# Optimization experiments

Measured on AMD Instinct MI355X. Metric: run time of the kernel, lower is better.

## Reference

```python
import jax, jax.numpy as jnp
import numpy as np

BSZ, IN_DIM, HID, OUT_DIM, N_ITERS = 262144, 64, 128, 64, 30


def setup_inputs() -> dict:
    key = jax.random.key(0)
    ks = jax.random.split(key, 6)
    s_h = 1.0 / np.sqrt(HID)
    s_i = 1.0 / np.sqrt(IN_DIM)
    return {
        "x": jax.random.normal(ks[0], (BSZ, IN_DIM), dtype=jnp.float32),
        "Wz": jax.random.uniform(ks[1], (HID, HID), jnp.float32, -s_h, s_h) * 0.9,  # scaled for contraction
        "Ux": jax.random.uniform(ks[2], (HID, IN_DIM), jnp.float32, -s_i, s_i),
        "b": jax.random.uniform(ks[3], (HID,), jnp.float32, -s_h, s_h),
        "Wd": jax.random.uniform(ks[4], (OUT_DIM, HID), jnp.float32, -s_h, s_h),
        "bd": jax.random.uniform(ks[5], (OUT_DIM,), jnp.float32, -s_h, s_h),
        "n_iters": N_ITERS,
    }


def reference(x, Wz, Ux, b, Wd, bd, n_iters):
    # injection term is iteration-invariant: compute once
    inj = x @ Ux.T + b                     # [B, HID]
    z0 = jnp.zeros((x.shape[0], Wz.shape[0]), dtype=x.dtype)

    def step(z, _):
        z = jax.nn.relu(z @ Wz.T + inj)    # f(z, x)
        return z, None

    z_star, _ = jax.lax.scan(step, z0, None, length=n_iters)
    return z_star @ Wd.T + bd              # decoder Linear
```

## Files before the change

### kernel.cpp

```cpp
#include <hip/hip_runtime.h>


typedef __attribute__((ext_vector_type(8))) __bf16 bf16x8;
typedef __attribute__((ext_vector_type(4))) __bf16 bf16x4;
typedef __attribute__((ext_vector_type(4))) float  floatx4;

#define MFMA16(a, b, c) __builtin_amdgcn_mfma_f32_16x16x32_bf16((a), (b), (c), 0, 0, 0)

static constexpr int kBsz = 262144;
static constexpr int kTM  = 64;

__device__ __forceinline__ bf16x8 cvt_bf16x8(float4 a, float4 b) {
  bf16x8 r;
  r[0] = (__bf16)a.x; r[1] = (__bf16)a.y; r[2] = (__bf16)a.z; r[3] = (__bf16)a.w;
  r[4] = (__bf16)b.x; r[5] = (__bf16)b.y; r[6] = (__bf16)b.z; r[7] = (__bf16)b.w;
  return r;
}

__global__ void __launch_bounds__(256) deq_fused(
    const float* __restrict__ x,
    const float* __restrict__ Wz,
    const float* __restrict__ Ux,
    const float* __restrict__ bvec,
    const float* __restrict__ Wd,
    const float* __restrict__ bd,
    const int*  __restrict__ n_iters_p,
    float* __restrict__ out)
{
  __shared__ __align__(16) __bf16 zl[2][kTM][136];

  const int tid  = threadIdx.x;
  const int lane = tid & 63;
  const int wv   = tid >> 6;
  const int wn   = wv & 1;
  const int wm   = wv >> 1;
  const int l15  = lane & 15;
  const int quad = lane >> 4;
  const int row0 = blockIdx.x * kTM;
  const int iters = *n_iters_p;

  bf16x8 awz[4][4];
#pragma unroll
  for (int nt = 0; nt < 4; ++nt) {
    const int n = 64 * wn + 16 * nt + l15;
#pragma unroll
    for (int ks = 0; ks < 4; ++ks) {
      const float4* p = (const float4*)(Wz + n * 128 + 32 * ks + 8 * quad);
      awz[nt][ks] = cvt_bf16x8(p[0], p[1]);
    }
  }

  floatx4 inj[4][2];
#pragma unroll
  for (int nt = 0; nt < 4; ++nt) {
    const float4 bv = *(const float4*)(bvec + 64 * wn + 16 * nt + 4 * quad);
#pragma unroll
    for (int mt = 0; mt < 2; ++mt) {
      floatx4 v = {bv.x, bv.y, bv.z, bv.w};
      inj[nt][mt] = v;
    }
  }
  {
    bf16x8 aux[4][2];
#pragma unroll
    for (int nt = 0; nt < 4; ++nt) {
      const int n = 64 * wn + 16 * nt + l15;
#pragma unroll
      for (int ks = 0; ks < 2; ++ks) {
        const float4* p = (const float4*)(Ux + n * 64 + 32 * ks + 8 * quad);
        aux[nt][ks] = cvt_bf16x8(p[0], p[1]);
      }
    }
#pragma unroll
    for (int mt = 0; mt < 2; ++mt) {
      const int m = row0 + 32 * wm + 16 * mt + l15;
#pragma unroll
      for (int ks = 0; ks < 2; ++ks) {
        const float4* p = (const float4*)(x + m * 64 + 32 * ks + 8 * quad);
        const bf16x8 bx = cvt_bf16x8(p[0], p[1]);
#pragma unroll
        for (int nt = 0; nt < 4; ++nt)
          inj[nt][mt] = MFMA16(aux[nt][ks], bx, inj[nt][mt]);
      }
    }
  }

#pragma unroll
  for (int mt = 0; mt < 2; ++mt) {
    const int ml = 32 * wm + 16 * mt + l15;
#pragma unroll
    for (int nt = 0; nt < 4; ++nt) {
      bf16x4 z4;
#pragma unroll
      for (int i = 0; i < 4; ++i) z4[i] = (__bf16)fmaxf(inj[nt][mt][i], 0.0f);
      *(bf16x4*)&zl[0][ml][64 * wn + 16 * nt + 4 * quad] = z4;
    }
  }

  int pb = 0;
  for (int t = 0; t < iters - 1; ++t) {
    __syncthreads();
    bf16x8 bz[2][4];
#pragma unroll
    for (int mt = 0; mt < 2; ++mt) {
      const int ml = 32 * wm + 16 * mt + l15;
#pragma unroll
      for (int ks = 0; ks < 4; ++ks)
        bz[mt][ks] = *(const bf16x8*)&zl[pb][ml][32 * ks + 8 * quad];
    }
    const int nb = pb ^ 1;
#pragma unroll
    for (int mt = 0; mt < 2; ++mt) {
      const int ml = 32 * wm + 16 * mt + l15;
#pragma unroll
      for (int nt = 0; nt < 4; ++nt) {
        floatx4 acc = inj[nt][mt];
#pragma unroll
        for (int ks = 0; ks < 4; ++ks)
          acc = MFMA16(awz[nt][ks], bz[mt][ks], acc);
        bf16x4 z4;
#pragma unroll
        for (int i = 0; i < 4; ++i) z4[i] = (__bf16)fmaxf(acc[i], 0.0f);
        *(bf16x4*)&zl[nb][ml][64 * wn + 16 * nt + 4 * quad] = z4;
      }
    }
    pb = nb;
  }
  __syncthreads();

  bf16x8 awd[2][4];
#pragma unroll
  for (int ot = 0; ot < 2; ++ot) {
    const int o = 32 * wn + 16 * ot + l15;
#pragma unroll
    for (int ks = 0; ks < 4; ++ks) {
      const float4* p = (const float4*)(Wd + o * 128 + 32 * ks + 8 * quad);
      awd[ot][ks] = cvt_bf16x8(p[0], p[1]);
    }
  }
#pragma unroll
  for (int mt = 0; mt < 2; ++mt) {
    const int ml = 32 * wm + 16 * mt + l15;
    bf16x8 bz[4];
#pragma unroll
    for (int ks = 0; ks < 4; ++ks)
      bz[ks] = *(const bf16x8*)&zl[pb][ml][32 * ks + 8 * quad];
#pragma unroll
    for (int ot = 0; ot < 2; ++ot) {
      const float4 bv = *(const float4*)(bd + 32 * wn + 16 * ot + 4 * quad);
      floatx4 acc = {bv.x, bv.y, bv.z, bv.w};
#pragma unroll
      for (int ks = 0; ks < 4; ++ks)
        acc = MFMA16(awd[ot][ks], bz[ks], acc);
      float4 ov;
      ov.x = acc[0]; ov.y = acc[1]; ov.z = acc[2]; ov.w = acc[3];
      *(float4*)(out + (size_t)(row0 + ml) * 64 + 32 * wn + 16 * ot + 4 * quad) = ov;
    }
  }
}

extern "C" void kernel_launch(void* const* d_in, const int* in_sizes, int n_in,
                              void* d_out, int out_size, void* d_ws, size_t ws_size,
                              hipStream_t stream) {
  const float* x  = (const float*)d_in[0];
  const float* Wz = (const float*)d_in[1];
  const float* Ux = (const float*)d_in[2];
  const float* b  = (const float*)d_in[3];
  const float* Wd = (const float*)d_in[4];
  const float* bd = (const float*)d_in[5];
  const int* n_it = (const int*)d_in[6];
  float* out = (float*)d_out;
  (void)in_sizes; (void)n_in; (void)d_ws; (void)ws_size; (void)out_size;

  dim3 grid(kBsz / kTM);
  deq_fused<<<grid, 256, 0, stream>>>(x, Wz, Ux, b, Wd, bd, n_it, out);
}
```

Before: 346.9 us.

## Keep DEQ state in registers per wave using permlane swaps instead of LDS

Each wave now owns 16 batch rows and the full 128-wide hidden state, so the iterate never leaves registers. The MFMA output layout is turned back into the B-operand layout with v_permlane32_swap and ds_swizzle, which removes the shared-memory round trip and the __syncthreads in each of the 30 iterations. In exchange each wave holds all of Wz in registers (32 bf16x8), which raises register pressure and may lower occupancy. It also gives up the 2x2 wave tiling in which each wave reused its Wz slice across 32 rows.

```diff
diff --git a/kernel.cpp b/kernel.cpp
--- a/kernel.cpp
+++ b/kernel.cpp
@@ -2,19 +2,46 @@
 
 
 typedef __attribute__((ext_vector_type(8))) __bf16 bf16x8;
-typedef __attribute__((ext_vector_type(4))) __bf16 bf16x4;
+typedef __attribute__((ext_vector_type(2))) __bf16 bf16x2;
 typedef __attribute__((ext_vector_type(4))) float  floatx4;
 
 #define MFMA16(a, b, c) __builtin_amdgcn_mfma_f32_16x16x32_bf16((a), (b), (c), 0, 0, 0)
 
 static constexpr int kBsz = 262144;
-static constexpr int kTM  = 64;
 
 __device__ __forceinline__ bf16x8 cvt_bf16x8(float4 a, float4 b) {
   bf16x8 r;
   r[0] = (__bf16)a.x; r[1] = (__bf16)a.y; r[2] = (__bf16)a.z; r[3] = (__bf16)a.w;
   r[4] = (__bf16)b.x; r[5] = (__bf16)b.y; r[6] = (__bf16)b.z; r[7] = (__bf16)b.w;
   return r;
+}
+
+__device__ __forceinline__ unsigned pk_relu2(float a, float b) {
+  union { bf16x2 h; unsigned u; } x;
+  x.h[0] = (__bf16)fmaxf(a, 0.0f);
+  x.h[1] = (__bf16)fmaxf(b, 0.0f);
+  return x.u;
+}
+
+union Frag { bf16x8 v; unsigned w[4]; };
+
+__device__ __forceinline__ bf16x8 build_frag(unsigned ulo, unsigned vlo,
+                                             unsigned uhi, unsigned vhi,
+                                             bool qodd) {
+  asm("v_permlane32_swap_b32 %0, %1" : "+v"(ulo), "+v"(vlo));
+  asm("v_permlane32_swap_b32 %0, %1" : "+v"(uhi), "+v"(vhi));
+  const unsigned c0 = qodd ? vlo : ulo;
+  const unsigned d0 = qodd ? ulo : vlo;
+  const unsigned c1 = qodd ? vhi : uhi;
+  const unsigned d1 = qodd ? uhi : vhi;
+  const unsigned dx0 = __builtin_amdgcn_ds_swizzle((int)d0, 0x401F);
+  const unsigned dx1 = __builtin_amdgcn_ds_swizzle((int)d1, 0x401F);
+  Frag f;
+  f.w[0] = qodd ? dx0 : c0;
+  f.w[1] = qodd ? dx1 : c1;
+  f.w[2] = qodd ? c0 : dx0;
+  f.w[3] = qodd ? c1 : dx1;
+  return f.v;
 }
 
 __global__ void __launch_bounds__(256) deq_fused(
@@ -27,135 +54,97 @@
     const int*  __restrict__ n_iters_p,
     float* __restrict__ out)
 {
-  __shared__ __align__(16) __bf16 zl[2][kTM][136];
-
   const int tid  = threadIdx.x;
   const int lane = tid & 63;
   const int wv   = tid >> 6;
-  const int wn   = wv & 1;
-  const int wm   = wv >> 1;
   const int l15  = lane & 15;
   const int quad = lane >> 4;
-  const int row0 = blockIdx.x * kTM;
-  const int iters = *n_iters_p;
+  const bool qodd = (quad & 1) != 0;
+  const int  mrow = blockIdx.x * 64 + wv * 16 + l15;
+  const int  iters = *n_iters_p;
 
-  bf16x8 awz[4][4];
+  floatx4 inj[8];
 #pragma unroll
-  for (int nt = 0; nt < 4; ++nt) {
-    const int n = 64 * wn + 16 * nt + l15;
-#pragma unroll
-    for (int ks = 0; ks < 4; ++ks) {
-      const float4* p = (const float4*)(Wz + n * 128 + 32 * ks + 8 * quad);
-      awz[nt][ks] = cvt_bf16x8(p[0], p[1]);
-    }
-  }
-
-  floatx4 inj[4][2];
-#pragma unroll
-  for (int nt = 0; nt < 4; ++nt) {
-    const float4 bv = *(const float4*)(bvec + 64 * wn + 16 * nt + 4 * quad);
-#pragma unroll
-    for (int mt = 0; mt < 2; ++mt) {
-      floatx4 v = {bv.x, bv.y, bv.z, bv.w};
-      inj[nt][mt] = v;
-    }
+  for (int t = 0; t < 8; ++t) {
+    const float4 bv = *(const float4*)(bvec + 16 * t + 4 * quad);
+    floatx4 v = {bv.x, bv.y, bv.z, bv.w};
+    inj[t] = v;
   }
   {
-    bf16x8 aux[4][2];
+    bf16x8 bx[2];
 #pragma unroll
-    for (int nt = 0; nt < 4; ++nt) {
-      const int n = 64 * wn + 16 * nt + l15;
+    for (int ks = 0; ks < 2; ++ks) {
+      const float4* p = (const float4*)(x + (size_t)mrow * 64 + 32 * ks + 8 * quad);
+      bx[ks] = cvt_bf16x8(p[0], p[1]);
+    }
+#pragma unroll
+    for (int t = 0; t < 8; ++t) {
 #pragma unroll
       for (int ks = 0; ks < 2; ++ks) {
-        const float4* p = (const float4*)(Ux + n * 64 + 32 * ks + 8 * quad);
-        aux[nt][ks] = cvt_bf16x8(p[0], p[1]);
-      }
-    }
-#pragma unroll
-    for (int mt = 0; mt < 2; ++mt) {
-      const int m = row0 + 32 * wm + 16 * mt + l15;
-#pragma unroll
-      for (int ks = 0; ks < 2; ++ks) {
-        const float4* p = (const float4*)(x + m * 64 + 32 * ks + 8 * quad);
-        const bf16x8 bx = cvt_bf16x8(p[0], p[1]);
-#pragma unroll
-        for (int nt = 0; nt < 4; ++nt)
-          inj[nt][mt] = MFMA16(aux[nt][ks], bx, inj[nt][mt]);
+        const float4* p = (const float4*)(Ux + (16 * t + l15) * 64 + 32 * ks + 8 * quad);
+        const bf16x8 a = cvt_bf16x8(p[0], p[1]);
+        inj[t] = MFMA16(a, bx[ks], inj[t]);
       }
     }
   }
 
+  bf16x8 awz[8][4];
 #pragma unroll
-  for (int mt = 0; mt < 2; ++mt) {
-    const int ml = 32 * wm + 16 * mt + l15;
+  for (int t = 0; t < 8; ++t)
 #pragma unroll
-    for (int nt = 0; nt < 4; ++nt) {
-      bf16x4 z4;
+    for (int ks = 0; ks < 4; ++ks) {
+      const float4* p = (const float4*)(Wz + (16 * t + l15) * 128 + 32 * ks + 8 * quad);
+      awz[t][ks] = cvt_bf16x8(p[0], p[1]);
+    }
+
+  unsigned lo[8], hi[8];
 #pragma unroll
-      for (int i = 0; i < 4; ++i) z4[i] = (__bf16)fmaxf(inj[nt][mt][i], 0.0f);
-      *(bf16x4*)&zl[0][ml][64 * wn + 16 * nt + 4 * quad] = z4;
+  for (int t = 0; t < 8; ++t) {
+    lo[t] = pk_relu2(inj[t][0], inj[t][1]);
+    hi[t] = pk_relu2(inj[t][2], inj[t][3]);
+  }
+
+  for (int it = 0; it < iters - 1; ++it) {
+    floatx4 acc[8];
+    {
+      const bf16x8 f0 = build_frag(lo[0], lo[1], hi[0], hi[1], qodd);
+#pragma unroll
+      for (int t = 0; t < 8; ++t)
+        acc[t] = MFMA16(awz[t][0], f0, inj[t]);
+    }
+#pragma unroll
+    for (int ks = 1; ks < 4; ++ks) {
+      const bf16x8 f = build_frag(lo[2 * ks], lo[2 * ks + 1],
+                                  hi[2 * ks], hi[2 * ks + 1], qodd);
+#pragma unroll
+      for (int t = 0; t < 8; ++t)
+        acc[t] = MFMA16(awz[t][ks], f, acc[t]);
+    }
+#pragma unroll
+    for (int t = 0; t < 8; ++t) {
+      lo[t] = pk_relu2(acc[t][0], acc[t][1]);
+      hi[t] = pk_relu2(acc[t][2], acc[t][3]);
     }
   }
 
-  int pb = 0;
-  for (int t = 0; t < iters - 1; ++t) {
-    __syncthreads();
-    bf16x8 bz[2][4];
+  bf16x8 bz[4];
 #pragma unroll
-    for (int mt = 0; mt < 2; ++mt) {
-      const int ml = 32 * wm + 16 * mt + l15;
+  for (int ks = 0; ks < 4; ++ks)
+    bz[ks] = build_frag(lo[2 * ks], lo[2 * ks + 1],
+                        hi[2 * ks], hi[2 * ks + 1], qodd);
 #pragma unroll
-      for (int ks = 0; ks < 4; ++ks)
-        bz[mt][ks] = *(const bf16x8*)&zl[pb][ml][32 * ks + 8 * quad];
-    }
-    const int nb = pb ^ 1;
-#pragma unroll
-    for (int mt = 0; mt < 2; ++mt) {
-      const int ml = 32 * wm + 16 * mt + l15;
-#pragma unroll
-      for (int nt = 0; nt < 4; ++nt) {
-        floatx4 acc = inj[nt][mt];
-#pragma unroll
-        for (int ks = 0; ks < 4; ++ks)
-          acc = MFMA16(awz[nt][ks], bz[mt][ks], acc);
-        bf16x4 z4;
-#pragma unroll
-        for (int i = 0; i < 4; ++i) z4[i] = (__bf16)fmaxf(acc[i], 0.0f);
-        *(bf16x4*)&zl[nb][ml][64 * wn + 16 * nt + 4 * quad] = z4;
-      }
-    }
-    pb = nb;
-  }
-  __syncthreads();
-
-  bf16x8 awd[2][4];
-#pragma unroll
-  for (int ot = 0; ot < 2; ++ot) {
-    const int o = 32 * wn + 16 * ot + l15;
+  for (int ot = 0; ot < 4; ++ot) {
+    const float4 bv = *(const float4*)(bd + 16 * ot + 4 * quad);
+    floatx4 acc = {bv.x, bv.y, bv.z, bv.w};
 #pragma unroll
     for (int ks = 0; ks < 4; ++ks) {
-      const float4* p = (const float4*)(Wd + o * 128 + 32 * ks + 8 * quad);
-      awd[ot][ks] = cvt_bf16x8(p[0], p[1]);
+      const float4* p = (const float4*)(Wd + (16 * ot + l15) * 128 + 32 * ks + 8 * quad);
+      const bf16x8 a = cvt_bf16x8(p[0], p[1]);
+      acc = MFMA16(a, bz[ks], acc);
     }
-  }
-#pragma unroll
-  for (int mt = 0; mt < 2; ++mt) {
-    const int ml = 32 * wm + 16 * mt + l15;
-    bf16x8 bz[4];
-#pragma unroll
-    for (int ks = 0; ks < 4; ++ks)
-      bz[ks] = *(const bf16x8*)&zl[pb][ml][32 * ks + 8 * quad];
-#pragma unroll
-    for (int ot = 0; ot < 2; ++ot) {
-      const float4 bv = *(const float4*)(bd + 32 * wn + 16 * ot + 4 * quad);
-      floatx4 acc = {bv.x, bv.y, bv.z, bv.w};
-#pragma unroll
-      for (int ks = 0; ks < 4; ++ks)
-        acc = MFMA16(awd[ot][ks], bz[ks], acc);
-      float4 ov;
-      ov.x = acc[0]; ov.y = acc[1]; ov.z = acc[2]; ov.w = acc[3];
-      *(float4*)(out + (size_t)(row0 + ml) * 64 + 32 * wn + 16 * ot + 4 * quad) = ov;
-    }
+    float4 ov;
+    ov.x = acc[0]; ov.y = acc[1]; ov.z = acc[2]; ov.w = acc[3];
+    *(float4*)(out + (size_t)mrow * 64 + 16 * ot + 4 * quad) = ov;
   }
 }
 
@@ -169,9 +158,9 @@
   const float* Wd = (const float*)d_in[4];
   const float* bd = (const float*)d_in[5];
   const int* n_it = (const int*)d_in[6];
-  float* out = (float*)d_out;
+  float* outp = (float*)d_out;
   (void)in_sizes; (void)n_in; (void)d_ws; (void)ws_size; (void)out_size;
 
-  dim3 grid(kBsz / kTM);
-  deq_fused<<<grid, 256, 0, stream>>>(x, Wz, Ux, b, Wd, bd, n_it, out);
+  dim3 grid(kBsz / 64);
+  deq_fused<<<grid, 256, 0, stream>>>(x, Wz, Ux, b, Wd, bd, n_it, outp);
 }
```

Result: slower. 603.6 us (+74.0%).

## Switch to 32x32x16 MFMA tiles with XOR-swizzled unpadded LDS layout

Applied to the files above, without the earlier changes.

Replaces the 16x16x32 bf16 MFMA tiling with 32x32x16 MFMA, so each wave holds a 32-row by 64-column output tile in two 16-element accumulators. LDS drops the padded 136-stride rows in favour of an unpadded 128 layout with an XOR swizzle on the row index to avoid bank conflicts. The larger MFMA shape means fewer instructions and fewer LDS reads of z per iteration, at the cost of changed register pressure and a different fragment layout for the stores.

```diff
diff --git a/kernel.cpp b/kernel.cpp
--- a/kernel.cpp
+++ b/kernel.cpp
@@ -1,11 +1,11 @@
 #include <hip/hip_runtime.h>
 
 
-typedef __attribute__((ext_vector_type(8))) __bf16 bf16x8;
-typedef __attribute__((ext_vector_type(4))) __bf16 bf16x4;
-typedef __attribute__((ext_vector_type(4))) float  floatx4;
+typedef __attribute__((ext_vector_type(8)))  __bf16 bf16x8;
+typedef __attribute__((ext_vector_type(4)))  __bf16 bf16x4;
+typedef __attribute__((ext_vector_type(16))) float  floatx16;
 
-#define MFMA16(a, b, c) __builtin_amdgcn_mfma_f32_16x16x32_bf16((a), (b), (c), 0, 0, 0)
+#define MFMA32(a, b, c) __builtin_amdgcn_mfma_f32_32x32x16_bf16((a), (b), (c), 0, 0, 0)
 
 static constexpr int kBsz = 262144;
 static constexpr int kTM  = 64;
@@ -27,135 +27,127 @@
     const int*  __restrict__ n_iters_p,
     float* __restrict__ out)
 {
-  __shared__ __align__(16) __bf16 zl[2][kTM][136];
+  __shared__ __align__(16) __bf16 zl[2][kTM * 128];
 
   const int tid  = threadIdx.x;
   const int lane = tid & 63;
   const int wv   = tid >> 6;
   const int wn   = wv & 1;
   const int wm   = wv >> 1;
-  const int l15  = lane & 15;
-  const int quad = lane >> 4;
+  const int l31  = lane & 31;
+  const int hi   = lane >> 5;
   const int row0 = blockIdx.x * kTM;
+  const int m    = 32 * wm + l31;
+  const int msw  = (m & 7) << 3;
   const int iters = *n_iters_p;
 
-  bf16x8 awz[4][4];
+  floatx16 inj[2];
 #pragma unroll
-  for (int nt = 0; nt < 4; ++nt) {
-    const int n = 64 * wn + 16 * nt + l15;
+  for (int nt = 0; nt < 2; ++nt)
+#pragma unroll
+    for (int g = 0; g < 4; ++g) {
+      const float4 bv = *(const float4*)(bvec + 64 * wn + 32 * nt + 8 * g + 4 * hi);
+      inj[nt][4 * g + 0] = bv.x; inj[nt][4 * g + 1] = bv.y;
+      inj[nt][4 * g + 2] = bv.z; inj[nt][4 * g + 3] = bv.w;
+    }
+  {
+    bf16x8 bx[4];
 #pragma unroll
     for (int ks = 0; ks < 4; ++ks) {
-      const float4* p = (const float4*)(Wz + n * 128 + 32 * ks + 8 * quad);
+      const float4* p = (const float4*)(x + (size_t)(row0 + m) * 64 + 16 * ks + 8 * hi);
+      bx[ks] = cvt_bf16x8(p[0], p[1]);
+    }
+#pragma unroll
+    for (int nt = 0; nt < 2; ++nt)
+#pragma unroll
+      for (int ks = 0; ks < 4; ++ks) {
+        const float4* p = (const float4*)(Ux + (64 * wn + 32 * nt + l31) * 64 + 16 * ks + 8 * hi);
+        inj[nt] = MFMA32(cvt_bf16x8(p[0], p[1]), bx[ks], inj[nt]);
+      }
+  }
+
+  bf16x8 awz[2][8];
+#pragma unroll
+  for (int nt = 0; nt < 2; ++nt)
+#pragma unroll
+    for (int ks = 0; ks < 8; ++ks) {
+      const float4* p = (const float4*)(Wz + (64 * wn + 32 * nt + l31) * 128 + 16 * ks + 8 * hi);
       awz[nt][ks] = cvt_bf16x8(p[0], p[1]);
     }
-  }
-
-  floatx4 inj[4][2];
-#pragma unroll
-  for (int nt = 0; nt < 4; ++nt) {
-    const float4 bv = *(const float4*)(bvec + 64 * wn + 16 * nt + 4 * quad);
-#pragma unroll
-    for (int mt = 0; mt < 2; ++mt) {
-      floatx4 v = {bv.x, bv.y, bv.z, bv.w};
-      inj[nt][mt] = v;
-    }
-  }
-  {
-    bf16x8 aux[4][2];
-#pragma unroll
-    for (int nt = 0; nt < 4; ++nt) {
-      const int n = 64 * wn + 16 * nt + l15;
-#pragma unroll
-      for (int ks = 0; ks < 2; ++ks) {
-        const float4* p = (const float4*)(Ux + n * 64 + 32 * ks + 8 * quad);
-        aux[nt][ks] = cvt_bf16x8(p[0], p[1]);
-      }
-    }
-#pragma unroll
-    for (int mt = 0; mt < 2; ++mt) {
-      const int m = row0 + 32 * wm + 16 * mt + l15;
-#pragma unroll
-      for (int ks = 0; ks < 2; ++ks) {
-        const float4* p = (const float4*)(x + m * 64 + 32 * ks + 8 * quad);
-        const bf16x8 bx = cvt_bf16x8(p[0], p[1]);
-#pragma unroll
-        for (int nt = 0; nt < 4; ++nt)
-          inj[nt][mt] = MFMA16(aux[nt][ks], bx, inj[nt][mt]);
-      }
-    }
-  }
 
 #pragma unroll
-  for (int mt = 0; mt < 2; ++mt) {
-    const int ml = 32 * wm + 16 * mt + l15;
+  for (int nt = 0; nt < 2; ++nt)
 #pragma unroll
-    for (int nt = 0; nt < 4; ++nt) {
+    for (int g = 0; g < 4; ++g) {
       bf16x4 z4;
 #pragma unroll
-      for (int i = 0; i < 4; ++i) z4[i] = (__bf16)fmaxf(inj[nt][mt][i], 0.0f);
-      *(bf16x4*)&zl[0][ml][64 * wn + 16 * nt + 4 * quad] = z4;
+      for (int i = 0; i < 4; ++i) z4[i] = (__bf16)fmaxf(inj[nt][4 * g + i], 0.0f);
+      const int n0 = 64 * wn + 32 * nt + 8 * g + 4 * hi;
+      *(bf16x4*)&zl[0][m * 128 + (n0 ^ msw)] = z4;
     }
-  }
 
   int pb = 0;
   for (int t = 0; t < iters - 1; ++t) {
     __syncthreads();
-    bf16x8 bz[2][4];
-#pragma unroll
-    for (int mt = 0; mt < 2; ++mt) {
-      const int ml = 32 * wm + 16 * mt + l15;
+    floatx16 acc[2];
+    acc[0] = inj[0]; acc[1] = inj[1];
+    {
+      bf16x8 bz[4];
 #pragma unroll
       for (int ks = 0; ks < 4; ++ks)
-        bz[mt][ks] = *(const bf16x8*)&zl[pb][ml][32 * ks + 8 * quad];
+        bz[ks] = *(const bf16x8*)&zl[pb][m * 128 + ((16 * ks + 8 * hi) ^ msw)];
+#pragma unroll
+      for (int nt = 0; nt < 2; ++nt)
+#pragma unroll
+        for (int ks = 0; ks < 4; ++ks)
+          acc[nt] = MFMA32(awz[nt][ks], bz[ks], acc[nt]);
+    }
+    {
+      bf16x8 bz[4];
+#pragma unroll
+      for (int ks = 0; ks < 4; ++ks)
+        bz[ks] = *(const bf16x8*)&zl[pb][m * 128 + ((16 * (ks + 4) + 8 * hi) ^ msw)];
+#pragma unroll
+      for (int nt = 0; nt < 2; ++nt)
+#pragma unroll
+        for (int ks = 0; ks < 4; ++ks)
+          acc[nt] = MFMA32(awz[nt][ks + 4], bz[ks], acc[nt]);
     }
     const int nb = pb ^ 1;
 #pragma unroll
-    for (int mt = 0; mt < 2; ++mt) {
-      const int ml = 32 * wm + 16 * mt + l15;
+    for (int nt = 0; nt < 2; ++nt)
 #pragma unroll
-      for (int nt = 0; nt < 4; ++nt) {
-        floatx4 acc = inj[nt][mt];
-#pragma unroll
-        for (int ks = 0; ks < 4; ++ks)
-          acc = MFMA16(awz[nt][ks], bz[mt][ks], acc);
+      for (int g = 0; g < 4; ++g) {
         bf16x4 z4;
 #pragma unroll
-        for (int i = 0; i < 4; ++i) z4[i] = (__bf16)fmaxf(acc[i], 0.0f);
-        *(bf16x4*)&zl[nb][ml][64 * wn + 16 * nt + 4 * quad] = z4;
+        for (int i = 0; i < 4; ++i) z4[i] = (__bf16)fmaxf(acc[nt][4 * g + i], 0.0f);
+        const int n0 = 64 * wn + 32 * nt + 8 * g + 4 * hi;
+        *(bf16x4*)&zl[nb][m * 128 + (n0 ^ msw)] = z4;
       }
-    }
     pb = nb;
   }
   __syncthreads();
 
-  bf16x8 awd[2][4];
+  floatx16 acc;
 #pragma unroll
-  for (int ot = 0; ot < 2; ++ot) {
-    const int o = 32 * wn + 16 * ot + l15;
-#pragma unroll
-    for (int ks = 0; ks < 4; ++ks) {
-      const float4* p = (const float4*)(Wd + o * 128 + 32 * ks + 8 * quad);
-      awd[ot][ks] = cvt_bf16x8(p[0], p[1]);
-    }
+  for (int g = 0; g < 4; ++g) {
+    const float4 bv = *(const float4*)(bd + 32 * wn + 8 * g + 4 * hi);
+    acc[4 * g + 0] = bv.x; acc[4 * g + 1] = bv.y;
+    acc[4 * g + 2] = bv.z; acc[4 * g + 3] = bv.w;
   }
 #pragma unroll
-  for (int mt = 0; mt < 2; ++mt) {
-    const int ml = 32 * wm + 16 * mt + l15;
-    bf16x8 bz[4];
+  for (int ks = 0; ks < 8; ++ks) {
+    const float4* p = (const float4*)(Wd + (32 * wn + l31) * 128 + 16 * ks + 8 * hi);
+    const bf16x8 a = cvt_bf16x8(p[0], p[1]);
+    const bf16x8 bzf = *(const bf16x8*)&zl[pb][m * 128 + ((16 * ks + 8 * hi) ^ msw)];
+    acc = MFMA32(a, bzf, acc);
+  }
 #pragma unroll
-    for (int ks = 0; ks < 4; ++ks)
-      bz[ks] = *(const bf16x8*)&zl[pb][ml][32 * ks + 8 * quad];
-#pragma unroll
-    for (int ot = 0; ot < 2; ++ot) {
-      const float4 bv = *(const float4*)(bd + 32 * wn + 16 * ot + 4 * quad);
-      floatx4 acc = {bv.x, bv.y, bv.z, bv.w};
-#pragma unroll
-      for (int ks = 0; ks < 4; ++ks)
-        acc = MFMA16(awd[ot][ks], bz[ks], acc);
-      float4 ov;
-      ov.x = acc[0]; ov.y = acc[1]; ov.z = acc[2]; ov.w = acc[3];
-      *(float4*)(out + (size_t)(row0 + ml) * 64 + 32 * wn + 16 * ot + 4 * quad) = ov;
-    }
+  for (int g = 0; g < 4; ++g) {
+    float4 ov;
+    ov.x = acc[4 * g + 0]; ov.y = acc[4 * g + 1];
+    ov.z = acc[4 * g + 2]; ov.w = acc[4 * g + 3];
+    *(float4*)(out + (size_t)(row0 + m) * 64 + 32 * wn + 8 * g + 4 * hi) = ov;
   }
 }
 
@@ -169,9 +161,9 @@
   const float* Wd = (const float*)d_in[4];
   const float* bd = (const float*)d_in[5];
   const int* n_it = (const int*)d_in[6];
-  float* out = (float*)d_out;
+  float* outp = (float*)d_out;
   (void)in_sizes; (void)n_in; (void)d_ws; (void)ws_size; (void)out_size;
 
   dim3 grid(kBsz / kTM);
-  deq_fused<<<grid, 256, 0, stream>>>(x, Wz, Ux, b, Wd, bd, n_it, out);
+  deq_fused<<<grid, 256, 0, stream>>>(x, Wz, Ux, b, Wd, bd, n_it, outp);
 }
```

After: 403.2 us. 16.3% more time.
